# Optimization experiments

Hardware: AMD Instinct MI355X
Metric: run time of the kernel (lower is better)

## Reference

```python
import jax, jax.numpy as jnp
import numpy as np

B, C_IN, C_OUT, H, W = 4, 256, 256, 56, 56
NH, K, P = 2, 5, 2
HD = C_OUT // NH          # 128
SE_H = C_OUT // 16        # 16
SE_H2 = max(SE_H // 16, 1)  # 1
EPS = 1e-5


def setup_inputs() -> dict:
    key = jax.random.key(0)
    ks = jax.random.split(key, 16)
    n = lambda k, sh, s=1.0: jax.random.normal(k, sh, jnp.float32) * s

    def bn_params(k, c):
        k1, k2 = jax.random.split(k)
        return (1.0 + 0.1 * n(k1, (c,)), 0.1 * n(k2, (c,)),
                jnp.zeros((c,), jnp.float32), jnp.ones((c,), jnp.float32))

    agg_g1, agg_b1, agg_m1, agg_v1 = bn_params(ks[6], C_OUT)
    agg_g2, agg_b2, agg_m2, agg_v2 = bn_params(ks[7], C_OUT)
    se_g_in, se_b_in, se_m_in, se_v_in = bn_params(ks[8], SE_H)
    se_g_out, se_b_out, se_m_out, se_v_out = bn_params(ks[9], C_OUT)
    return {
        "x": n(ks[0], (B, C_IN, H, W)),
        "Wq": n(ks[1], (C_OUT, C_IN), C_IN ** -0.5),
        "Wk": n(ks[2], (C_OUT, C_IN), C_IN ** -0.5),
        "Wv": n(ks[3], (C_OUT, C_IN), C_IN ** -0.5),
        "rel_h": n(ks[4], (HD, 1, 1, K, 1)),
        "rel_w": n(ks[5], (HD, 1, 1, 1, K)),
        "agg_g1": agg_g1, "agg_b1": agg_b1, "agg_m1": agg_m1, "agg_v1": agg_v1,
        "agg_W": n(ks[10], (C_OUT, C_OUT), C_OUT ** -0.5),
        "agg_g2": agg_g2, "agg_b2": agg_b2, "agg_m2": agg_m2, "agg_v2": agg_v2,
        "se_Win": n(ks[11], (SE_H, C_OUT), C_OUT ** -0.5),
        "se_g_in": se_g_in, "se_b_in": se_b_in, "se_m_in": se_m_in, "se_v_in": se_v_in,
        "se_fc1": n(ks[12], (SE_H2, SE_H), SE_H ** -0.5),
        "se_fc2": n(ks[13], (SE_H, SE_H2)),
        "se_Wout": n(ks[14], (C_OUT, SE_H), SE_H ** -0.5),
        "se_g_out": se_g_out, "se_b_out": se_b_out, "se_m_out": se_m_out, "se_v_out": se_v_out,
    }


def _conv1x1(Wm, t):
    return jnp.einsum('oc,bchw->bohw', Wm, t)


def _bn(t, g, b, m, v):
    # eval-mode BatchNorm2d with running stats
    return (t - m[:, None, None]) * (g * jax.lax.rsqrt(v + EPS))[:, None, None] + b[:, None, None]


def _windows(t):
    # (B, O, H+2P, W+2P) -> (B, O, H, W, K, K), matching torch unfold(2,K,1).unfold(3,K,1)
    w = jnp.stack([t[:, :, i:i + H, j:j + W] for i in range(K) for j in range(K)], axis=-1)
    return w.reshape(t.shape[0], t.shape[1], H, W, K, K)


def reference(x, Wq, Wk, Wv, rel_h, rel_w,
              agg_g1, agg_b1, agg_m1, agg_v1, agg_W, agg_g2, agg_b2, agg_m2, agg_v2,
              se_Win, se_g_in, se_b_in, se_m_in, se_v_in, se_fc1, se_fc2, se_Wout,
              se_g_out, se_b_out, se_m_out, se_v_out):
    xp = jnp.pad(x, ((0, 0), (0, 0), (P, P), (P, P)))
    q = _conv1x1(Wq, x).reshape(B, NH, HD, H, W)          # (B,NH,HD,H,W)
    k_win = _windows(_conv1x1(Wk, xp))                    # (B,O,H,W,K,K)
    v_win = _windows(_conv1x1(Wv, xp))
    # relative position bias: first head gets rel_h (height taps), second gets rel_w
    k_win = jnp.concatenate([k_win[:, :HD] + rel_h[None], k_win[:, HD:] + rel_w[None]], axis=1)
    k_r = k_win.reshape(B, NH, HD, H, W, K * K)
    v_r = v_win.reshape(B, NH, HD, H, W, K * K)
    scores = jnp.einsum('bnchw,bnchwk->bnhwk', q, k_r) / jnp.sqrt(jnp.float32(HD))
    attn = jax.nn.softmax(scores, axis=-1)
    out = jnp.einsum('bnhwk,bnchwk->bnchw', attn, v_r).reshape(B, C_OUT, H, W)
    # agg: BN -> ReLU -> 1x1 conv -> BN
    y = jax.nn.relu(_bn(out, agg_g1, agg_b1, agg_m1, agg_v1))
    y = _bn(_conv1x1(agg_W, y), agg_g2, agg_b2, agg_m2, agg_v2)
    # squeeze-excitation (intended math; original view(b,c) is a channel-count bug)
    s = jax.nn.relu(_bn(_conv1x1(se_Win, y), se_g_in, se_b_in, se_m_in, se_v_in))  # (B,SE_H,H,W)
    p = s.mean(axis=(2, 3))                                                        # (B,SE_H)
    g = jax.nn.sigmoid(jax.nn.relu(p @ se_fc1.T) @ se_fc2.T)                       # (B,SE_H)
    s = s * g[:, :, None, None]
    return _bn(_conv1x1(se_Wout, s), se_g_out, se_b_out, se_m_out, se_v_out)
```

## Files before the change

### kernel.cpp

```cpp
#include <hip/hip_runtime.h>
#include <hip/hip_bf16.h>

#define HW 3136
#define HH 56
#define WW 56
#define BB 4
#define CC 256
#define HD 128

#define TH 4
#define TW 8
#define WR 8
#define WC 12
#define WPX 96
#define KSTR 132
#define SSTR 33

#define ASTR 72

typedef __attribute__((ext_vector_type(8))) short bf16x8;
typedef __attribute__((ext_vector_type(4))) float f32x4;

__device__ __forceinline__ unsigned short f2bf(float f) {
    unsigned int u; __builtin_memcpy(&u, &f, 4);
    unsigned int r = u + 0x7FFFu + ((u >> 16) & 1u);
    return (unsigned short)(r >> 16);
}

__global__ __launch_bounds__(256) void xt_cvt(const float* __restrict__ x,
                                              unsigned short* __restrict__ xt)
{
    int b = blockIdx.z;
    int c0 = blockIdx.y * 64;
    int p0 = blockIdx.x * 64;
    __shared__ float tile[64][65];
    int t = threadIdx.x;
    int p4 = t & 15, cl = t >> 4;
    const float* xb = x + ((size_t)b * CC + c0) * HW + p0;
#pragma unroll
    for (int i = 0; i < 4; i++) {
        int c = cl + 16 * i;
        float4 f = *(const float4*)(xb + (size_t)c * HW + p4 * 4);
        tile[c][p4 * 4 + 0] = f.x; tile[c][p4 * 4 + 1] = f.y;
        tile[c][p4 * 4 + 2] = f.z; tile[c][p4 * 4 + 3] = f.w;
    }
    __syncthreads();
    int c2 = t & 31, pl = t >> 5;
    unsigned short* xo = xt + ((size_t)b * HW + p0) * CC + c0;
#pragma unroll
    for (int i = 0; i < 8; i++) {
        int p = pl + 8 * i;
        float a = tile[2 * c2][p], bb = tile[2 * c2 + 1][p];
        unsigned int pk = (unsigned int)f2bf(a) | ((unsigned int)f2bf(bb) << 16);
        *(unsigned int*)(xo + (size_t)p * CC + 2 * c2) = pk;
    }
}

__global__ __launch_bounds__(256) void wcvt(const float* __restrict__ Wq,
                                            const float* __restrict__ Wk,
                                            const float* __restrict__ Wv,
                                            const float* __restrict__ Wa,
                                            unsigned short* __restrict__ wb)
{
    const float* srcs[4] = {Wq, Wk, Wv, Wa};
    const float* s = srcs[blockIdx.y];
    int idx = blockIdx.x * 256 + threadIdx.x;
    float4 f = *(const float4*)(s + (size_t)idx * 4);
    uint2 pk;
    pk.x = (unsigned int)f2bf(f.x) | ((unsigned int)f2bf(f.y) << 16);
    pk.y = (unsigned int)f2bf(f.z) | ((unsigned int)f2bf(f.w) << 16);
    *(uint2*)(wb + (size_t)blockIdx.y * 65536 + (size_t)idx * 4) = pk;
}

__global__ __launch_bounds__(256) void qkv_mfma(
    const unsigned short* __restrict__ xt, const unsigned short* __restrict__ wqkv,
    float* __restrict__ q_ws, float* __restrict__ k_ws, float* __restrict__ v_ws)
{
    int wsel = blockIdx.z;
    float* outp = (wsel == 0) ? q_ws : ((wsel == 1) ? k_ws : v_ws);
    int gp0 = blockIdx.x * 128, o0 = blockIdx.y * 128;

    __shared__ unsigned short As[128 * ASTR];
    __shared__ unsigned short Bs[128 * ASTR];
    const unsigned short* xb = xt + (size_t)gp0 * CC;
    const unsigned short* wbp = wqkv + (size_t)wsel * 65536 + (size_t)o0 * CC;

    int t = threadIdx.x;
    int wave = t >> 6, lane = t & 63;
    int mo = (wave & 1) * 64, no = (wave >> 1) * 64;
    int lm = lane & 15, lq = lane >> 4;
    int sr = t >> 3, sc = t & 7;

    f32x4 acc[4][4];
#pragma unroll
    for (int i = 0; i < 4; i++)
#pragma unroll
        for (int j = 0; j < 4; j++) acc[i][j] = (f32x4){0.f, 0.f, 0.f, 0.f};

    for (int k0 = 0; k0 < 256; k0 += 64) {
#pragma unroll
        for (int i = 0; i < 4; i++) {
            int r = sr + 32 * i;
            *(uint4*)&As[r * ASTR + sc * 8] = *(const uint4*)(xb + (size_t)r * CC + k0 + sc * 8);
            *(uint4*)&Bs[r * ASTR + sc * 8] = *(const uint4*)(wbp + (size_t)r * CC + k0 + sc * 8);
        }
        __syncthreads();
#pragma unroll
        for (int ks = 0; ks < 64; ks += 32) {
            bf16x8 af[4], bfr[4];
#pragma unroll
            for (int i = 0; i < 4; i++)
                af[i] = *(bf16x8*)&As[(mo + 16 * i + lm) * ASTR + ks + lq * 8];
#pragma unroll
            for (int j = 0; j < 4; j++)
                bfr[j] = *(bf16x8*)&Bs[(no + 16 * j + lm) * ASTR + ks + lq * 8];
#pragma unroll
            for (int i = 0; i < 4; i++)
#pragma unroll
                for (int j = 0; j < 4; j++)
                    acc[i][j] = __builtin_amdgcn_mfma_f32_16x16x32_bf16(
                        af[i], bfr[j], acc[i][j], 0, 0, 0);
        }
        __syncthreads();
    }
    float* ob = outp + (size_t)gp0 * CC + o0;
#pragma unroll
    for (int i = 0; i < 4; i++)
#pragma unroll
        for (int j = 0; j < 4; j++)
#pragma unroll
            for (int r = 0; r < 4; r++) {
                int m = mo + 16 * i + lq * 4 + r;
                int n = no + 16 * j + lm;
                ob[(size_t)m * CC + n] = acc[i][j][r];
            }
}

__global__ __launch_bounds__(256) void agg_mfma(
    const float* __restrict__ ao, const unsigned short* __restrict__ wagg,
    const float* __restrict__ g1, const float* __restrict__ b1,
    const float* __restrict__ m1, const float* __restrict__ v1,
    const float* __restrict__ g2, const float* __restrict__ b2,
    const float* __restrict__ m2, const float* __restrict__ v2,
    float* __restrict__ y2)
{
    int gp0 = blockIdx.x * 128, o0 = blockIdx.y * 128;

    __shared__ unsigned short As[128 * ASTR];
    __shared__ unsigned short Bs[128 * ASTR];
    __shared__ float s1[256], o1[256], s2[256], o2[256];

    int t = threadIdx.x;
    {
        float sc1 = g1[t] * rsqrtf(v1[t] + 1e-5f);
        s1[t] = sc1; o1[t] = b1[t] - m1[t] * sc1;
        float sc2 = g2[t] * rsqrtf(v2[t] + 1e-5f);
        s2[t] = sc2; o2[t] = b2[t] - m2[t] * sc2;
    }

    const float* aob = ao + (size_t)gp0 * CC;
    const unsigned short* wbp = wagg + (size_t)o0 * CC;

    int wave = t >> 6, lane = t & 63;
    int mo = (wave & 1) * 64, no = (wave >> 1) * 64;
    int lm = lane & 15, lq = lane >> 4;
    int sr = t >> 3, sc = t & 7;

    f32x4 acc[4][4];
#pragma unroll
    for (int i = 0; i < 4; i++)
#pragma unroll
        for (int j = 0; j < 4; j++) acc[i][j] = (f32x4){0.f, 0.f, 0.f, 0.f};

    __syncthreads();

    for (int k0 = 0; k0 < 256; k0 += 64) {
#pragma unroll
        for (int i = 0; i < 4; i++) {
            int r = sr + 32 * i;
            int cb = k0 + sc * 8;
            const float* arow = aob + (size_t)r * CC + cb;
            float4 f0 = *(const float4*)(arow);
            float4 f1 = *(const float4*)(arow + 4);
            float e[8] = {f0.x, f0.y, f0.z, f0.w, f1.x, f1.y, f1.z, f1.w};
            unsigned short pk[8];
#pragma unroll
            for (int u = 0; u < 8; u++) {
                float vv = fmaxf(e[u] * s1[cb + u] + o1[cb + u], 0.f);
                pk[u] = f2bf(vv);
            }
            *(uint4*)&As[r * ASTR + sc * 8] = *(uint4*)pk;
            *(uint4*)&Bs[r * ASTR + sc * 8] = *(const uint4*)(wbp + (size_t)r * CC + k0 + sc * 8);
        }
        __syncthreads();
#pragma unroll
        for (int ks = 0; ks < 64; ks += 32) {
            bf16x8 af[4], bfr[4];
#pragma unroll
            for (int i = 0; i < 4; i++)
                af[i] = *(bf16x8*)&As[(mo + 16 * i + lm) * ASTR + ks + lq * 8];
#pragma unroll
            for (int j = 0; j < 4; j++)
                bfr[j] = *(bf16x8*)&Bs[(no + 16 * j + lm) * ASTR + ks + lq * 8];
#pragma unroll
            for (int i = 0; i < 4; i++)
#pragma unroll
                for (int j = 0; j < 4; j++)
                    acc[i][j] = __builtin_amdgcn_mfma_f32_16x16x32_bf16(
                        af[i], bfr[j], acc[i][j], 0, 0, 0);
        }
        __syncthreads();
    }
    float* yb = y2 + (size_t)gp0 * CC + o0;
#pragma unroll
    for (int i = 0; i < 4; i++)
#pragma unroll
        for (int j = 0; j < 4; j++)
#pragma unroll
            for (int r = 0; r < 4; r++) {
                int m = mo + 16 * i + lq * 4 + r;
                int n = no + 16 * j + lm;
                yb[(size_t)m * CC + n] = acc[i][j][r] * s2[o0 + n] + o2[o0 + n];
            }
}

__global__ __launch_bounds__(256) void attn_kernel(
    const float* __restrict__ q_ws, const float* __restrict__ k_ws,
    const float* __restrict__ v_ws,
    const float* __restrict__ rel_h, const float* __restrict__ rel_w,
    float* __restrict__ ao_ws)
{
    __shared__ float kwin[WPX * KSTR];
    __shared__ float sbuf[32 * SSTR];
    __shared__ float relT[5 * KSTR];

    int t = threadIdx.x;
    int tile = blockIdx.x;
    int n = blockIdx.y;
    int b = blockIdx.z;
    int tr = tile / 7, tc = tile - tr * 7;
    int h0 = tr * TH, w0 = tc * TW;
    const float* rel = (n == 0) ? rel_h : rel_w;
    const size_t base = (size_t)b * HW * CC + n * HD;

    {
        int c4 = t & 31, pw0 = t >> 5;
#pragma unroll
        for (int it = 0; it < 12; it++) {
            int pw = pw0 + it * 8;
            int wr = pw / 12, wc = pw - wr * 12;
            int gh = h0 + wr - 2, gw = w0 + wc - 2;
            float4 f = make_float4(0.f, 0.f, 0.f, 0.f);
            if (gh >= 0 && gh < HH && gw >= 0 && gw < WW)
                f = *(const float4*)(k_ws + base + (size_t)(gh * WW + gw) * CC + c4 * 4);
            *(float4*)&kwin[pw * KSTR + c4 * 4] = f;
        }
        if (t < 128) {
#pragma unroll
            for (int tt = 0; tt < 5; tt++)
                relT[tt * KSTR + t] = rel[t * 5 + tt];
        }
    }
    __syncthreads();

    int px = t >> 3, c4g = t & 7;
    int pr = px >> 3, pc = px & 7;
    int ghp = h0 + pr, gwp = w0 + pc;
    const size_t pbase = base + (size_t)(ghp * WW + gwp) * CC;

    float4 q4[4];
#pragma unroll
    for (int i = 0; i < 4; i++)
        q4[i] = *(const float4*)(q_ws + pbase + (c4g + 8 * i) * 4);

    float acc[30];
#pragma unroll
    for (int tt = 0; tt < 30; tt++) acc[tt] = 0.f;
#pragma unroll
    for (int i = 0; i < 4; i++) {
        float4 q = q4[i];
        int co = (c4g + 8 * i) * 4;
#pragma unroll
        for (int tt = 0; tt < 25; tt++) {
            int di = tt / 5, dj = tt - 5 * (tt / 5);
            int wpx = (pr + di) * WC + pc + dj;
            float4 k4 = *(const float4*)&kwin[wpx * KSTR + co];
            acc[tt] += q.x * k4.x + q.y * k4.y + q.z * k4.z + q.w * k4.w;
        }
#pragma unroll
        for (int tt = 0; tt < 5; tt++) {
            float4 r4 = *(const float4*)&relT[tt * KSTR + co];
            acc[25 + tt] += q.x * r4.x + q.y * r4.y + q.z * r4.z + q.w * r4.w;
        }
    }
#pragma unroll
    for (int tt = 0; tt < 30; tt++) {
#pragma unroll
        for (int m = 1; m < 8; m <<= 1)
            acc[tt] += __shfl_xor(acc[tt], m, 64);
    }
#pragma unroll
    for (int tt = 0; tt < 30; tt++)
        if ((tt & 7) == c4g) sbuf[px * SSTR + tt] = acc[tt];
    __syncthreads();

    {
        int c4 = t & 31, pw0 = t >> 5;
#pragma unroll
        for (int it = 0; it < 12; it++) {
            int pw = pw0 + it * 8;
            int wr = pw / 12, wc = pw - wr * 12;
            int gh = h0 + wr - 2, gw = w0 + wc - 2;
            float4 f = make_float4(0.f, 0.f, 0.f, 0.f);
            if (gh >= 0 && gh < HH && gw >= 0 && gw < WW)
                f = *(const float4*)(v_ws + base + (size_t)(gh * WW + gw) * CC + c4 * 4);
            *(float4*)&kwin[pw * KSTR + c4 * 4] = f;
        }
    }
    if (t < 32) {
        float s[25], b5[5];
#pragma unroll
        for (int tt = 0; tt < 25; tt++) s[tt] = sbuf[t * SSTR + tt];
#pragma unroll
        for (int tt = 0; tt < 5; tt++) b5[tt] = sbuf[t * SSTR + 25 + tt];
        const float inv = 0.08838834764831845f;
        float mx = -1e30f;
#pragma unroll
        for (int tt = 0; tt < 25; tt++) {
            int di = tt / 5, dj = tt - 5 * (tt / 5);
            s[tt] = (s[tt] + ((n == 0) ? b5[di] : b5[dj])) * inv;
            mx = fmaxf(mx, s[tt]);
        }
        float sum = 0.f;
#pragma unroll
        for (int tt = 0; tt < 25; tt++) { s[tt] = __expf(s[tt] - mx); sum += s[tt]; }
        float rs = 1.f / sum;
#pragma unroll
        for (int tt = 0; tt < 25; tt++) sbuf[t * SSTR + tt] = s[tt] * rs;
    }
    __syncthreads();

    float w25[25];
#pragma unroll
    for (int tt = 0; tt < 25; tt++) w25[tt] = sbuf[px * SSTR + tt];
    float4 oacc[4];
#pragma unroll
    for (int i = 0; i < 4; i++) oacc[i] = make_float4(0.f, 0.f, 0.f, 0.f);
#pragma unroll
    for (int tt = 0; tt < 25; tt++) {
        int di = tt / 5, dj = tt - 5 * (tt / 5);
        int wpx = (pr + di) * WC + pc + dj;
        float a = w25[tt];
#pragma unroll
        for (int i = 0; i < 4; i++) {
            float4 v4 = *(const float4*)&kwin[wpx * KSTR + (c4g + 8 * i) * 4];
            oacc[i].x += a * v4.x; oacc[i].y += a * v4.y;
            oacc[i].z += a * v4.z; oacc[i].w += a * v4.w;
        }
    }
#pragma unroll
    for (int i = 0; i < 4; i++)
        *(float4*)(ao_ws + pbase + (c4g + 8 * i) * 4) = oacc[i];
}

__global__ __launch_bounds__(256) void se_in_kernel(
    const float* __restrict__ y2, const float* __restrict__ se_Win,
    const float* __restrict__ gin, const float* __restrict__ bin,
    const float* __restrict__ min_, const float* __restrict__ vin,
    float* __restrict__ s_ws, float* __restrict__ psum)
{
    int b = blockIdx.y;
    int p0 = blockIdx.x * 16;
    __shared__ float yt[16][257];
    __shared__ float wt[16][257];
    __shared__ float red[16][17];
    int t = threadIdx.x;
    const float* yb = y2 + (size_t)(b * HW + p0) * CC;
#pragma unroll
    for (int i = 0; i < 16; i++) yt[i][t] = yb[(size_t)i * CC + t];
#pragma unroll
    for (int i = 0; i < 16; i++) wt[i][t] = se_Win[i * 256 + t];
    __syncthreads();
    int p = t >> 4, j = t & 15;
    float dot = 0.f;
#pragma unroll 8
    for (int c = 0; c < 256; c++) dot += yt[p][c] * wt[j][c];
    float sc = gin[j] * rsqrtf(vin[j] + 1e-5f);
    float sv = fmaxf((dot - min_[j]) * sc + bin[j], 0.f);
    s_ws[(size_t)(b * HW + p0 + p) * 16 + j] = sv;
    red[p][j] = sv;
    __syncthreads();
    if (t < 16) {
        float sm = 0.f;
#pragma unroll
        for (int pp = 0; pp < 16; pp++) sm += red[pp][t];
        atomicAdd(&psum[b * 16 + t], sm);
    }
}

__global__ void zero64(float* p) { p[threadIdx.x] = 0.f; }

__global__ void se_gate(const float* __restrict__ psum,
                        const float* __restrict__ fc1,
                        const float* __restrict__ fc2,
                        float* __restrict__ g_ws)
{
    int t = threadIdx.x;
    if (t >= 64) return;
    int b = t >> 4, j = t & 15;
    float h = 0.f;
#pragma unroll
    for (int jj = 0; jj < 16; jj++)
        h += (psum[b * 16 + jj] * (1.f / 3136.f)) * fc1[jj];
    h = fmaxf(h, 0.f);
    float z = h * fc2[j];
    g_ws[t] = 1.f / (1.f + __expf(-z));
}

__global__ __launch_bounds__(256) void se_out_kernel(
    const float* __restrict__ s_ws, const float* __restrict__ g_ws,
    const float* __restrict__ se_Wout,
    const float* __restrict__ gout, const float* __restrict__ bout,
    const float* __restrict__ mout, const float* __restrict__ vout,
    float* __restrict__ out)
{
    int b = blockIdx.z;
    int o0 = blockIdx.y * 4;
    int p0 = blockIdx.x * 64;
    __shared__ float st[64][17];
    __shared__ float wg[4][16];
    int t = threadIdx.x;
#pragma unroll
    for (int i = 0; i < 4; i++) {
        int idx = i * 256 + t;
        st[idx >> 4][idx & 15] = s_ws[(size_t)(b * HW + p0 + (idx >> 4)) * 16 + (idx & 15)];
    }
    if (t < 64) {
        int ol = t >> 4, j = t & 15;
        wg[ol][j] = se_Wout[(o0 + ol) * 16 + j] * g_ws[b * 16 + j];
    }
    __syncthreads();
    int ol = t >> 6, pl = t & 63;
    float dot = 0.f;
#pragma unroll
    for (int j = 0; j < 16; j++) dot += st[pl][j] * wg[ol][j];
    int o = o0 + ol;
    float sc = gout[o] * rsqrtf(vout[o] + 1e-5f);
    float r = (dot - mout[o]) * sc + bout[o];
    out[((size_t)(b * 256 + o)) * HW + p0 + pl] = r;
}

extern "C" void kernel_launch(void* const* d_in, const int* in_sizes, int n_in,
                              void* d_out, int out_size, void* d_ws, size_t ws_size,
                              hipStream_t stream) {
    const float* x     = (const float*)d_in[0];
    const float* Wq    = (const float*)d_in[1];
    const float* Wk    = (const float*)d_in[2];
    const float* Wv    = (const float*)d_in[3];
    const float* rel_h = (const float*)d_in[4];
    const float* rel_w = (const float*)d_in[5];
    const float* agg_g1 = (const float*)d_in[6];
    const float* agg_b1 = (const float*)d_in[7];
    const float* agg_m1 = (const float*)d_in[8];
    const float* agg_v1 = (const float*)d_in[9];
    const float* agg_W  = (const float*)d_in[10];
    const float* agg_g2 = (const float*)d_in[11];
    const float* agg_b2 = (const float*)d_in[12];
    const float* agg_m2 = (const float*)d_in[13];
    const float* agg_v2 = (const float*)d_in[14];
    const float* se_Win = (const float*)d_in[15];
    const float* se_g_in = (const float*)d_in[16];
    const float* se_b_in = (const float*)d_in[17];
    const float* se_m_in = (const float*)d_in[18];
    const float* se_v_in = (const float*)d_in[19];
    const float* se_fc1  = (const float*)d_in[20];
    const float* se_fc2  = (const float*)d_in[21];
    const float* se_Wout = (const float*)d_in[22];
    const float* se_g_out = (const float*)d_in[23];
    const float* se_b_out = (const float*)d_in[24];
    const float* se_m_out = (const float*)d_in[25];
    const float* se_v_out = (const float*)d_in[26];

    float* ws = (float*)d_ws;
    const size_t NQ = (size_t)BB * HW * CC;
    float* q_ws = ws;
    float* k_ws = q_ws + NQ;
    float* v_ws = k_ws + NQ;
    float* ao_ws = v_ws + NQ;
    float* y2_ws = q_ws;
    unsigned short* xt = (unsigned short*)ao_ws;
    float* s_ws = ao_ws + NQ;
    float* psum = s_ws + (size_t)BB * HW * 16;
    float* g_ws = psum + 64;
    unsigned short* wbf = (unsigned short*)(g_ws + 64);

    xt_cvt<<<dim3(49, 4, 4), 256, 0, stream>>>(x, xt);
    wcvt<<<dim3(64, 4), 256, 0, stream>>>(Wq, Wk, Wv, agg_W, wbf);
    qkv_mfma<<<dim3(98, 2, 3), 256, 0, stream>>>(xt, wbf, q_ws, k_ws, v_ws);
    attn_kernel<<<dim3(98, 2, 4), 256, 0, stream>>>(q_ws, k_ws, v_ws, rel_h, rel_w, ao_ws);
    agg_mfma<<<dim3(98, 2), 256, 0, stream>>>(ao_ws, wbf + 3 * 65536,
        agg_g1, agg_b1, agg_m1, agg_v1, agg_g2, agg_b2, agg_m2, agg_v2, y2_ws);
    zero64<<<1, 64, 0, stream>>>(psum);
    se_in_kernel<<<dim3(196, 4), 256, 0, stream>>>(y2_ws, se_Win,
        se_g_in, se_b_in, se_m_in, se_v_in, s_ws, psum);
    se_gate<<<1, 64, 0, stream>>>(psum, se_fc1, se_fc2, g_ws);
    se_out_kernel<<<dim3(49, 64, 4), 256, 0, stream>>>(s_ws, g_ws, se_Wout,
        se_g_out, se_b_out, se_m_out, se_v_out, (float*)d_out);
}
```

Measured before the change: 213.2 us.

## Store Q/K/V and attention output intermediates as bf16 instead of fp32

The QKV GEMM now writes bf16, packing neighbouring columns through a lane shuffle. The attention kernel reads bf16 K/V/Q and widens them to fp32 in shared memory, then writes its output as bf16 for the aggregation GEMM. This halves global traffic for the largest intermediates and removes a bf16 round trip that the aggregation GEMM did anyway. The cost is lower precision for Q/K/V and the attention output, extra conversion ALU work, and a workspace layout where y2 aliases the bf16 q/k region.

```diff
diff --git a/kernel.cpp b/kernel.cpp
--- a/kernel.cpp
+++ b/kernel.cpp
@@ -25,6 +25,12 @@
     unsigned int u; __builtin_memcpy(&u, &f, 4);
     unsigned int r = u + 0x7FFFu + ((u >> 16) & 1u);
     return (unsigned short)(r >> 16);
+}
+__device__ __forceinline__ float bflo(unsigned int u) {
+    unsigned int x = u << 16; float f; __builtin_memcpy(&f, &x, 4); return f;
+}
+__device__ __forceinline__ float bfhi(unsigned int u) {
+    unsigned int x = u & 0xFFFF0000u; float f; __builtin_memcpy(&f, &x, 4); return f;
 }
 
 __global__ __launch_bounds__(256) void xt_cvt(const float* __restrict__ x,
@@ -74,10 +80,11 @@
 
 __global__ __launch_bounds__(256) void qkv_mfma(
     const unsigned short* __restrict__ xt, const unsigned short* __restrict__ wqkv,
-    float* __restrict__ q_ws, float* __restrict__ k_ws, float* __restrict__ v_ws)
+    unsigned short* __restrict__ q_ws, unsigned short* __restrict__ k_ws,
+    unsigned short* __restrict__ v_ws)
 {
     int wsel = blockIdx.z;
-    float* outp = (wsel == 0) ? q_ws : ((wsel == 1) ? k_ws : v_ws);
+    unsigned short* outp = (wsel == 0) ? q_ws : ((wsel == 1) ? k_ws : v_ws);
     int gp0 = blockIdx.x * 128, o0 = blockIdx.y * 128;
 
     __shared__ unsigned short As[128 * ASTR];
@@ -123,21 +130,30 @@
         }
         __syncthreads();
     }
-    float* ob = outp + (size_t)gp0 * CC + o0;
+    unsigned short* ob = outp + (size_t)gp0 * CC + o0;
+    bool ev = (lm & 1) == 0;
+    int elm = lm & ~1;
 #pragma unroll
     for (int i = 0; i < 4; i++)
 #pragma unroll
         for (int j = 0; j < 4; j++)
 #pragma unroll
             for (int r = 0; r < 4; r++) {
-                int m = mo + 16 * i + lq * 4 + r;
-                int n = no + 16 * j + lm;
-                ob[(size_t)m * CC + n] = acc[i][j][r];
+                float v = acc[i][j][r];
+                float p = __shfl_xor(v, 1, 64);
+                unsigned int pk = ev
+                    ? ((unsigned int)f2bf(v) | ((unsigned int)f2bf(p) << 16))
+                    : ((unsigned int)f2bf(p) | ((unsigned int)f2bf(v) << 16));
+                if (ev == (r < 2)) {
+                    int m = mo + 16 * i + lq * 4 + r;
+                    int n = no + 16 * j + elm;
+                    *(unsigned int*)(ob + (size_t)m * CC + n) = pk;
+                }
             }
 }
 
 __global__ __launch_bounds__(256) void agg_mfma(
-    const float* __restrict__ ao, const unsigned short* __restrict__ wagg,
+    const unsigned short* __restrict__ ao, const unsigned short* __restrict__ wagg,
     const float* __restrict__ g1, const float* __restrict__ b1,
     const float* __restrict__ m1, const float* __restrict__ v1,
     const float* __restrict__ g2, const float* __restrict__ b2,
@@ -158,7 +174,7 @@
         s2[t] = sc2; o2[t] = b2[t] - m2[t] * sc2;
     }
 
-    const float* aob = ao + (size_t)gp0 * CC;
+    const unsigned short* aob = ao + (size_t)gp0 * CC;
     const unsigned short* wbp = wagg + (size_t)o0 * CC;
 
     int wave = t >> 6, lane = t & 63;
@@ -179,15 +195,14 @@
         for (int i = 0; i < 4; i++) {
             int r = sr + 32 * i;
             int cb = k0 + sc * 8;
-            const float* arow = aob + (size_t)r * CC + cb;
-            float4 f0 = *(const float4*)(arow);
-            float4 f1 = *(const float4*)(arow + 4);
-            float e[8] = {f0.x, f0.y, f0.z, f0.w, f1.x, f1.y, f1.z, f1.w};
+            uint4 u = *(const uint4*)(aob + (size_t)r * CC + cb);
+            float e[8] = {bflo(u.x), bfhi(u.x), bflo(u.y), bfhi(u.y),
+                          bflo(u.z), bfhi(u.z), bflo(u.w), bfhi(u.w)};
             unsigned short pk[8];
 #pragma unroll
-            for (int u = 0; u < 8; u++) {
-                float vv = fmaxf(e[u] * s1[cb + u] + o1[cb + u], 0.f);
-                pk[u] = f2bf(vv);
+            for (int uu = 0; uu < 8; uu++) {
+                float vv = fmaxf(e[uu] * s1[cb + uu] + o1[cb + uu], 0.f);
+                pk[uu] = f2bf(vv);
             }
             *(uint4*)&As[r * ASTR + sc * 8] = *(uint4*)pk;
             *(uint4*)&Bs[r * ASTR + sc * 8] = *(const uint4*)(wbp + (size_t)r * CC + k0 + sc * 8);
@@ -225,10 +240,10 @@
 }
 
 __global__ __launch_bounds__(256) void attn_kernel(
-    const float* __restrict__ q_ws, const float* __restrict__ k_ws,
-    const float* __restrict__ v_ws,
+    const unsigned short* __restrict__ q_ws, const unsigned short* __restrict__ k_ws,
+    const unsigned short* __restrict__ v_ws,
     const float* __restrict__ rel_h, const float* __restrict__ rel_w,
-    float* __restrict__ ao_ws)
+    unsigned short* __restrict__ ao_ws)
 {
     __shared__ float kwin[WPX * KSTR];
     __shared__ float sbuf[32 * SSTR];
@@ -244,16 +259,20 @@
     const size_t base = (size_t)b * HW * CC + n * HD;
 
     {
-        int c4 = t & 31, pw0 = t >> 5;
-#pragma unroll
-        for (int it = 0; it < 12; it++) {
-            int pw = pw0 + it * 8;
+        int c8 = t & 15, pw0 = t >> 4;
+#pragma unroll
+        for (int it = 0; it < 6; it++) {
+            int pw = pw0 + it * 16;
             int wr = pw / 12, wc = pw - wr * 12;
             int gh = h0 + wr - 2, gw = w0 + wc - 2;
-            float4 f = make_float4(0.f, 0.f, 0.f, 0.f);
-            if (gh >= 0 && gh < HH && gw >= 0 && gw < WW)
-                f = *(const float4*)(k_ws + base + (size_t)(gh * WW + gw) * CC + c4 * 4);
-            *(float4*)&kwin[pw * KSTR + c4 * 4] = f;
+            float f[8] = {0.f, 0.f, 0.f, 0.f, 0.f, 0.f, 0.f, 0.f};
+            if (gh >= 0 && gh < HH && gw >= 0 && gw < WW) {
+                uint4 u = *(const uint4*)(k_ws + base + (size_t)(gh * WW + gw) * CC + c8 * 8);
+                f[0] = bflo(u.x); f[1] = bfhi(u.x); f[2] = bflo(u.y); f[3] = bfhi(u.y);
+                f[4] = bflo(u.z); f[5] = bfhi(u.z); f[6] = bflo(u.w); f[7] = bfhi(u.w);
+            }
+            *(float4*)&kwin[pw * KSTR + c8 * 8]     = make_float4(f[0], f[1], f[2], f[3]);
+            *(float4*)&kwin[pw * KSTR + c8 * 8 + 4] = make_float4(f[4], f[5], f[6], f[7]);
         }
         if (t < 128) {
 #pragma unroll
@@ -270,8 +289,10 @@
 
     float4 q4[4];
 #pragma unroll
-    for (int i = 0; i < 4; i++)
-        q4[i] = *(const float4*)(q_ws + pbase + (c4g + 8 * i) * 4);
+    for (int i = 0; i < 4; i++) {
+        uint2 uq = *(const uint2*)(q_ws + pbase + (c4g + 8 * i) * 4);
+        q4[i] = make_float4(bflo(uq.x), bfhi(uq.x), bflo(uq.y), bfhi(uq.y));
+    }
 
     float acc[30];
 #pragma unroll
@@ -305,16 +326,20 @@
     __syncthreads();
 
     {
-        int c4 = t & 31, pw0 = t >> 5;
-#pragma unroll
-        for (int it = 0; it < 12; it++) {
-            int pw = pw0 + it * 8;
+        int c8 = t & 15, pw0 = t >> 4;
+#pragma unroll
+        for (int it = 0; it < 6; it++) {
+            int pw = pw0 + it * 16;
             int wr = pw / 12, wc = pw - wr * 12;
             int gh = h0 + wr - 2, gw = w0 + wc - 2;
-            float4 f = make_float4(0.f, 0.f, 0.f, 0.f);
-            if (gh >= 0 && gh < HH && gw >= 0 && gw < WW)
-                f = *(const float4*)(v_ws + base + (size_t)(gh * WW + gw) * CC + c4 * 4);
-            *(float4*)&kwin[pw * KSTR + c4 * 4] = f;
+            float f[8] = {0.f, 0.f, 0.f, 0.f, 0.f, 0.f, 0.f, 0.f};
+            if (gh >= 0 && gh < HH && gw >= 0 && gw < WW) {
+                uint4 u = *(const uint4*)(v_ws + base + (size_t)(gh * WW + gw) * CC + c8 * 8);
+                f[0] = bflo(u.x); f[1] = bfhi(u.x); f[2] = bflo(u.y); f[3] = bfhi(u.y);
+                f[4] = bflo(u.z); f[5] = bfhi(u.z); f[6] = bflo(u.w); f[7] = bfhi(u.w);
+            }
+            *(float4*)&kwin[pw * KSTR + c8 * 8]     = make_float4(f[0], f[1], f[2], f[3]);
+            *(float4*)&kwin[pw * KSTR + c8 * 8 + 4] = make_float4(f[4], f[5], f[6], f[7]);
         }
     }
     if (t < 32) {
@@ -359,8 +384,12 @@
         }
     }
 #pragma unroll
-    for (int i = 0; i < 4; i++)
-        *(float4*)(ao_ws + pbase + (c4g + 8 * i) * 4) = oacc[i];
+    for (int i = 0; i < 4; i++) {
+        uint2 pk;
+        pk.x = (unsigned int)f2bf(oacc[i].x) | ((unsigned int)f2bf(oacc[i].y) << 16);
+        pk.y = (unsigned int)f2bf(oacc[i].z) | ((unsigned int)f2bf(oacc[i].w) << 16);
+        *(uint2*)(ao_ws + pbase + (c4g + 8 * i) * 4) = pk;
+    }
 }
 
 __global__ __launch_bounds__(256) void se_in_kernel(
@@ -481,17 +510,16 @@
     const float* se_m_out = (const float*)d_in[25];
     const float* se_v_out = (const float*)d_in[26];
 
-    float* ws = (float*)d_ws;
     const size_t NQ = (size_t)BB * HW * CC;
-    float* q_ws = ws;
-    float* k_ws = q_ws + NQ;
-    float* v_ws = k_ws + NQ;
-    float* ao_ws = v_ws + NQ;
-    float* y2_ws = q_ws;
-    unsigned short* xt = (unsigned short*)ao_ws;
-    float* s_ws = ao_ws + NQ;
-    float* psum = s_ws + (size_t)BB * HW * 16;
-    float* g_ws = psum + 64;
+    unsigned short* q_ws  = (unsigned short*)d_ws;
+    unsigned short* k_ws  = q_ws + NQ;
+    unsigned short* v_ws  = k_ws + NQ;
+    unsigned short* ao_ws = v_ws + NQ;
+    unsigned short* xt    = ao_ws;
+    float* y2_ws = (float*)d_ws;
+    float* s_ws  = (float*)(ao_ws + NQ);
+    float* psum  = s_ws + (size_t)BB * HW * 16;
+    float* g_ws  = psum + 64;
     unsigned short* wbf = (unsigned short*)(g_ws + 64);
 
     xt_cvt<<<dim3(49, 4, 4), 256, 0, stream>>>(x, xt);
```

New measurement: 206.6 us. 1.03x faster.
